# Kernel optimization log

Measured on AMD Instinct MI355X. Metric: run time of the kernel, lower is better.

## Reference

```python
import jax, jax.numpy as jnp
import numpy as np

D_MODEL = 1024
M = 50
B, N = 8, 4096
NOISE_P = 0.0464
TEMP = 0.1
EPS = 1e-12


def _l2norm(v):
    return v / jnp.clip(jnp.linalg.norm(v, axis=-1, keepdims=True), EPS)


def setup_inputs() -> dict:
    key = jax.random.key(0)
    ks = jax.random.split(key, 8)
    x = jax.random.normal(ks[0], (B, N, D_MODEL), dtype=jnp.float32)
    prime_nodes = jax.random.normal(ks[1], (M, D_MODEL), dtype=jnp.float32)
    w_cov = jnp.float32(1.0)
    w_hyd = jnp.float32(0.5)
    w_vdw = jnp.float32(0.1)
    A_cov = jnp.asarray(np.roll(np.eye(M, dtype=np.float32), 1, axis=0))
    A_hyd = jnp.asarray(np.tril(np.ones((M, M), dtype=np.float32), k=-1))
    A_vdw = jax.random.normal(ks[2], (M, M), dtype=jnp.float32) * 0.05
    # expert MLP: Linear(D,4D) -> GELU -> Linear(4D,D); kaiming-uniform-ish init
    lim1 = 1.0 / np.sqrt(D_MODEL)
    lim2 = 1.0 / np.sqrt(4 * D_MODEL)
    W1 = jax.random.uniform(ks[3], (D_MODEL, 4 * D_MODEL), minval=-lim1, maxval=lim1, dtype=jnp.float32)
    b1 = jax.random.uniform(ks[4], (4 * D_MODEL,), minval=-lim1, maxval=lim1, dtype=jnp.float32)
    W2 = jax.random.uniform(ks[5], (4 * D_MODEL, D_MODEL), minval=-lim2, maxval=lim2, dtype=jnp.float32)
    b2 = jax.random.uniform(ks[6], (D_MODEL,), minval=-lim2, maxval=lim2, dtype=jnp.float32)
    return {"x": x, "prime_nodes": prime_nodes, "w_cov": w_cov, "w_hyd": w_hyd,
            "w_vdw": w_vdw, "A_cov": A_cov, "A_hyd": A_hyd, "A_vdw": A_vdw,
            "W1": W1, "b1": b1, "W2": W2, "b2": b2}


def reference(x, prime_nodes, w_cov, w_hyd, w_vdw, A_cov, A_hyd, A_vdw, W1, b1, W2, b2):
    # soft codebook routing: cosine-sim softmax over M primes, temperature 0.1
    C = jax.nn.softmax(jnp.einsum('bnd,md->bnm', _l2norm(x), _l2norm(prime_nodes)) / TEMP, axis=-1)
    H_prime = jnp.einsum('bnm,bnd->bmd', C, x)  # (B, M, D)
    A = jax.nn.softmax(w_cov * A_cov + w_hyd * A_hyd + w_vdw * A_vdw, axis=-1)
    # einsum('mn,bmd->bmd', A, H_prime): n only appears in A -> rowsum scaling
    H = A.sum(axis=1)[None, :, None] * H_prime
    # single latent step (latent_steps=1 default)
    U, _, Vt = jnp.linalg.svd(H, full_matrices=False)  # U:(B,M,M), Vt:(B,M,D)
    H_logic = jnp.einsum('bij,bjd->bid', U, Vt)  # orthogonal (polar) factor
    nk1, nk2 = jax.random.split(jax.random.key(42))
    mask = (jax.random.uniform(nk1, H_logic.shape) < NOISE_P).astype(H_logic.dtype)
    noise = jax.random.normal(nk2, H_logic.shape, dtype=H_logic.dtype) * 0.1
    z = H_logic + mask * noise
    h = jax.nn.gelu(z @ W1 + b1, approximate=False)
    H = jnp.tanh(h @ W2 + b2)
    # residual decode back to tokens (continuous_mode=False)
    return x + jnp.einsum('bnm,bmd->bnd', C, H)
```

## Files before the change

### kernel.cpp

```cpp
#include <hip/hip_runtime.h>
#include <stdint.h>
#include <math.h>

#define NS_ITERS 26
#define PIT 72
#define P2  72

typedef unsigned short u16;
typedef __attribute__((ext_vector_type(8))) short short8;
typedef __attribute__((ext_vector_type(4))) float f32x4;

__device__ __forceinline__ u16 f2b(float f){
  unsigned u = __float_as_uint(f);
  unsigned r = (u + 0x7FFFu + ((u>>16)&1u)) >> 16;
  return (u16)r;
}
__device__ __forceinline__ float b2f(u16 h){ return __uint_as_float(((unsigned)h)<<16); }
__device__ __forceinline__ unsigned pk2(float lo, float hi){
  return (unsigned)f2b(lo) | ((unsigned)f2b(hi) << 16);
}

__host__ __device__ constexpr uint32_t rotl32(uint32_t v, int n){ return (v<<n)|(v>>(32-n)); }
struct TFOut { uint32_t a, b; };
__host__ __device__ constexpr TFOut tf2x32(uint32_t k0, uint32_t k1, uint32_t x0, uint32_t x1){
  uint32_t ks2 = k0 ^ k1 ^ 0x1BD11BDAu;
  x0 += k0; x1 += k1;
#define TFR(R) x0 += x1; x1 = rotl32(x1,(R)) ^ x0;
  TFR(13) TFR(15) TFR(26) TFR(6)
  x0 += k1; x1 += ks2 + 1u;
  TFR(17) TFR(29) TFR(16) TFR(24)
  x0 += ks2; x1 += k0 + 2u;
  TFR(13) TFR(15) TFR(26) TFR(6)
  x0 += k0; x1 += k1 + 3u;
  TFR(17) TFR(29) TFR(16) TFR(24)
  x0 += k1; x1 += ks2 + 4u;
  TFR(13) TFR(15) TFR(26) TFR(6)
  x0 += ks2; x1 += k0 + 5u;
#undef TFR
  return TFOut{x0, x1};
}

__device__ __forceinline__ float erfinv_f32(float x){
  float w = -log1pf(-x*x);
  float p;
  if (w < 5.0f) {
    w -= 2.5f;
    p = 2.81022636e-08f;
    p = fmaf(p, w, 3.43273939e-07f);
    p = fmaf(p, w, -3.5233877e-06f);
    p = fmaf(p, w, -4.39150654e-06f);
    p = fmaf(p, w, 0.00021858087f);
    p = fmaf(p, w, -0.00125372503f);
    p = fmaf(p, w, -0.00417768164f);
    p = fmaf(p, w, 0.246640727f);
    p = fmaf(p, w, 1.50140941f);
  } else {
    w = sqrtf(w) - 3.0f;
    p = -0.000200214257f;
    p = fmaf(p, w, 0.000100950558f);
    p = fmaf(p, w, 0.00134934322f);
    p = fmaf(p, w, -0.00367342844f);
    p = fmaf(p, w, 0.00573950773f);
    p = fmaf(p, w, -0.0076224613f);
    p = fmaf(p, w, 0.00943887047f);
    p = fmaf(p, w, 1.00167406f);
    p = fmaf(p, w, 2.83297682f);
  }
  return p * x;
}

__global__ __launch_bounds__(256) void kprepAll(const float* __restrict__ prime, u16* __restrict__ PT,
                                                const float* __restrict__ W1, u16* __restrict__ W1T,
                                                const float* __restrict__ W2, u16* __restrict__ W2T){
  int blk = blockIdx.x;
  int tid = threadIdx.x;
  if (blk < 64){
    int m = blk;
    u16* dst = PT + m*1024;
    if (m >= 50){ for (int k = tid; k < 1024; k += 256) dst[k] = 0; return; }
    __shared__ float red[256];
    const float* pr = prime + m*1024;
    float ss = 0.f;
    for (int k = tid; k < 1024; k += 256){ float v = pr[k]; ss = fmaf(v,v,ss); }
    red[tid] = ss; __syncthreads();
    for (int s = 128; s > 0; s >>= 1){ if (tid < s) red[tid] += red[tid+s]; __syncthreads(); }
    float sc = 1.0f / fmaxf(sqrtf(red[0]), 1e-12f);
    for (int k = tid; k < 1024; k += 256) dst[k] = f2b(pr[k]*sc);
    return;
  }
  const float* src; u16* dst; int srcStride, dstStride;
  if (blk < 1088){
    int t = blk - 64;
    int kt2 = t >> 6, nt2 = t & 63;
    src = W1 + (size_t)(kt2*64)*4096 + nt2*64; srcStride = 4096;
    dst = W1T + (size_t)(nt2*64)*1024 + kt2*64; dstStride = 1024;
  } else {
    int t = blk - 1088;
    int kt2 = t >> 4, dt2 = t & 15;
    src = W2 + (size_t)(kt2*64)*1024 + dt2*64; srcStride = 1024;
    dst = W2T + (size_t)(dt2*64)*4096 + kt2*64; dstStride = 4096;
  }
  __shared__ __align__(16) u16 ts[64*PIT];
  int r = tid>>2, sseg = tid&3;
  {
    const float* s0 = src + (size_t)r*srcStride + sseg*16;
    unsigned p[8];
#pragma unroll
    for (int i = 0; i < 4; i++){
      float4 v = *reinterpret_cast<const float4*>(s0 + i*4);
      p[2*i]   = pk2(v.x, v.y);
      p[2*i+1] = pk2(v.z, v.w);
    }
    uint4 w0; w0.x=p[0]; w0.y=p[1]; w0.z=p[2]; w0.w=p[3];
    uint4 w1; w1.x=p[4]; w1.y=p[5]; w1.z=p[6]; w1.w=p[7];
    *reinterpret_cast<uint4*>(&ts[r*PIT + sseg*16])     = w0;
    *reinterpret_cast<uint4*>(&ts[r*PIT + sseg*16 + 8]) = w1;
  }
  __syncthreads();
  {
    int n2 = tid>>2, kseg = tid&3;
    unsigned q[8];
#pragma unroll
    for (int j = 0; j < 8; j++){
      u16 lo = ts[(kseg*16 + 2*j)*PIT + n2];
      u16 hi = ts[(kseg*16 + 2*j+1)*PIT + n2];
      q[j] = (unsigned)lo | ((unsigned)hi<<16);
    }
    u16* d2 = dst + (size_t)n2*dstStride + kseg*16;
    uint4 w0; w0.x=q[0]; w0.y=q[1]; w0.z=q[2]; w0.w=q[3];
    uint4 w1; w1.x=q[4]; w1.y=q[5]; w1.z=q[6]; w1.w=q[7];
    *reinterpret_cast<uint4*>(d2)   = w0;
    *reinterpret_cast<uint4*>(d2+8) = w1;
  }
}

__global__ __launch_bounds__(256) void kC(const float* __restrict__ x, const u16* __restrict__ PT,
                                          u16* __restrict__ C, u16* __restrict__ CT){
  int blk = blockIdx.x; int b = blk>>6, n0 = (blk&63)<<6;
  int tid = threadIdx.x, lane = tid&63, w = tid>>6;
  __shared__ __align__(16) u16 xs[64*PIT];
  __shared__ __align__(16) u16 ps[64*PIT];
  __shared__ float sq[64][5];
  f32x4 acc[4] = {{0,0,0,0},{0,0,0,0},{0,0,0,0},{0,0,0,0}};
  float sqa = 0.f;
  int stok = tid>>2, sseg = tid&3;
  int qtok = tid&63, qg = tid>>6;
  const float* xb = x + ((size_t)(b*4096 + n0))*1024;
  for (int kc = 0; kc < 16; kc++){
    int k0 = kc*64;
    __syncthreads();
    {
      const float* src = xb + (size_t)stok*1024 + k0 + sseg*16;
      unsigned p[8];
#pragma unroll
      for (int i = 0; i < 4; i++){
        float4 v = *reinterpret_cast<const float4*>(src + i*4);
        p[2*i]   = pk2(v.x, v.y);
        p[2*i+1] = pk2(v.z, v.w);
      }
      uint4 w0; w0.x=p[0]; w0.y=p[1]; w0.z=p[2]; w0.w=p[3];
      uint4 w1; w1.x=p[4]; w1.y=p[5]; w1.z=p[6]; w1.w=p[7];
      *reinterpret_cast<uint4*>(&xs[stok*PIT + sseg*16])     = w0;
      *reinterpret_cast<uint4*>(&xs[stok*PIT + sseg*16 + 8]) = w1;
    }
    {
      const u16* src = PT + (size_t)stok*1024 + k0 + sseg*16;
      *reinterpret_cast<uint4*>(&ps[stok*PIT + sseg*16])   = *reinterpret_cast<const uint4*>(src);
      *reinterpret_cast<uint4*>(&ps[stok*PIT + sseg*16+8]) = *reinterpret_cast<const uint4*>(src+8);
    }
    __syncthreads();
    {
      const u16* xr = &xs[qtok*PIT + qg*16];
#pragma unroll
      for (int j = 0; j < 16; j++){ float v = b2f(xr[j]); sqa = fmaf(v,v,sqa); }
    }
#pragma unroll
    for (int s = 0; s < 2; s++){
      short8 a = *reinterpret_cast<const short8*>(&xs[(16*w + (lane&15))*PIT + s*32 + (lane>>4)*8]);
#pragma unroll
      for (int t = 0; t < 4; t++){
        short8 bb = *reinterpret_cast<const short8*>(&ps[(t*16 + (lane&15))*PIT + s*32 + (lane>>4)*8]);
        acc[t] = __builtin_amdgcn_mfma_f32_16x16x32_bf16(a, bb, acc[t], 0, 0, 0);
      }
    }
  }
  sq[qtok][qg] = sqa;
  __syncthreads();
  if (tid < 64){
    float ss = sq[tid][0]+sq[tid][1]+sq[tid][2]+sq[tid][3];
    sq[tid][4] = 10.0f / fmaxf(sqrtf(ss), 1e-12f);
  }
  __syncthreads();
  u16* cl = xs;
#pragma unroll
  for (int r = 0; r < 4; r++){
    int gt = 16*w + (lane>>4)*4 + r;
    float scale = sq[gt][4];
    float v[4];
#pragma unroll
    for (int t = 0; t < 4; t++) v[t] = acc[t][r] * scale;
    if ((lane&15) >= 2) v[3] = -1e30f;
    float mx = fmaxf(fmaxf(v[0],v[1]), fmaxf(v[2],v[3]));
#pragma unroll
    for (int off = 1; off < 16; off <<= 1) mx = fmaxf(mx, __shfl_xor(mx, off, 64));
    float e[4], sum = 0.f;
#pragma unroll
    for (int t = 0; t < 4; t++){ e[t] = __expf(v[t]-mx); sum += e[t]; }
#pragma unroll
    for (int off = 1; off < 16; off <<= 1) sum += __shfl_xor(sum, off, 64);
    float inv = 1.0f / sum;
#pragma unroll
    for (int t = 0; t < 4; t++) cl[gt*PIT + t*16 + (lane&15)] = f2b(e[t]*inv);
  }
  __syncthreads();
  {
    u16* dst = C + ((size_t)(b*4096 + n0 + stok))*64 + sseg*16;
    *reinterpret_cast<uint4*>(dst)   = *reinterpret_cast<const uint4*>(&cl[stok*PIT + sseg*16]);
    *reinterpret_cast<uint4*>(dst+8) = *reinterpret_cast<const uint4*>(&cl[stok*PIT + sseg*16+8]);
  }
  {
    int m = tid>>2, nseg = tid&3;
    unsigned vs[8];
#pragma unroll
    for (int j = 0; j < 8; j++){
      u16 lo = cl[(nseg*16 + 2*j)*PIT + m];
      u16 hi = cl[(nseg*16 + 2*j+1)*PIT + m];
      vs[j] = (unsigned)lo | ((unsigned)hi<<16);
    }
    u16* dst = CT + ((size_t)(b*64 + m))*4096 + n0 + nseg*16;
    uint4 w0; w0.x=vs[0]; w0.y=vs[1]; w0.z=vs[2]; w0.w=vs[3];
    uint4 w1; w1.x=vs[4]; w1.y=vs[5]; w1.z=vs[6]; w1.w=vs[7];
    *reinterpret_cast<uint4*>(dst)   = w0;
    *reinterpret_cast<uint4*>(dst+8) = w1;
  }
}

__global__ __launch_bounds__(256) void kHp2(const float* __restrict__ x, const u16* __restrict__ CT,
                                            float* __restrict__ Hpart){
  int blk = blockIdx.x;
  int kt = blk & 3, dt = (blk >> 2) & 15, b = blk >> 6;
  int d0 = dt*64;
  int tid = threadIdx.x, lane = tid&63, w = tid>>6;
  __shared__ __align__(16) u16 cs[64*PIT];
  __shared__ __align__(16) u16 xt[64*PIT];
  f32x4 acc[4] = {{0,0,0,0},{0,0,0,0},{0,0,0,0},{0,0,0,0}};
  int nn = tid>>2, seg = tid&3;
  int np = tid & 31, dsg = tid >> 5;
  for (int nc = 0; nc < 16; nc++){
    int n0 = kt*1024 + nc*64;
    __syncthreads();
    {
      const u16* src = CT + ((size_t)(b*64 + nn))*4096 + n0 + seg*16;
      *reinterpret_cast<uint4*>(&cs[nn*PIT + seg*16])   = *reinterpret_cast<const uint4*>(src);
      *reinterpret_cast<uint4*>(&cs[nn*PIT + seg*16+8]) = *reinterpret_cast<const uint4*>(src+8);
    }
    {
      const float* s0 = x + ((size_t)(b*4096 + n0 + 2*np))*1024 + d0 + dsg*8;
      const float* s1 = s0 + 1024;
      float4 a0 = *reinterpret_cast<const float4*>(s0);
      float4 a1 = *reinterpret_cast<const float4*>(s0+4);
      float4 c0v = *reinterpret_cast<const float4*>(s1);
      float4 c1v = *reinterpret_cast<const float4*>(s1+4);
      float av[8] = {a0.x,a0.y,a0.z,a0.w,a1.x,a1.y,a1.z,a1.w};
      float cv[8] = {c0v.x,c0v.y,c0v.z,c0v.w,c1v.x,c1v.y,c1v.z,c1v.w};
#pragma unroll
      for (int j2 = 0; j2 < 8; j2++){
        int dd = dsg*8 + j2;
        *reinterpret_cast<unsigned*>(&xt[dd*PIT + 2*np]) = pk2(av[j2], cv[j2]);
      }
    }
    __syncthreads();
#pragma unroll
    for (int s = 0; s < 2; s++){
      short8 a = *reinterpret_cast<const short8*>(&cs[(16*w + (lane&15))*PIT + s*32 + (lane>>4)*8]);
#pragma unroll
      for (int t = 0; t < 4; t++){
        short8 bb = *reinterpret_cast<const short8*>(&xt[(t*16 + (lane&15))*PIT + s*32 + (lane>>4)*8]);
        acc[t] = __builtin_amdgcn_mfma_f32_16x16x32_bf16(a, bb, acc[t], 0, 0, 0);
      }
    }
  }
#pragma unroll
  for (int t = 0; t < 4; t++)
#pragma unroll
    for (int r = 0; r < 4; r++){
      int m = 16*w + (lane>>4)*4 + r;
      int d = d0 + t*16 + (lane&15);
      if (m < 50) Hpart[(((size_t)(b*4) + kt)*50 + m)*1024 + d] = acc[t][r];
    }
}

__global__ void kredH(const float* __restrict__ Hpart, float* __restrict__ H, u16* __restrict__ Hb){
  int e = blockIdx.x*256 + threadIdx.x;
  int b = e >> 16, rem = e & 65535;
  int m = rem >> 10, d = rem & 1023;
  size_t o = ((size_t)(b*64 + m))*1024 + d;
  if (m < 50){
    const float* p = Hpart + (size_t)b*204800 + m*1024 + d;
    float s = p[0] + p[51200] + p[102400] + p[153600];
    H[o] = s;
    Hb[o] = f2b(s);
  } else {
    Hb[o] = 0;
  }
}

__global__ __launch_bounds__(256) void kgram(const u16* __restrict__ Hb, float* __restrict__ G){
  int b = blockIdx.x;
  int tid = threadIdx.x, lane = tid&63, w = tid>>6;
  __shared__ __align__(16) u16 hs[64*PIT];
  f32x4 acc[4] = {{0,0,0,0},{0,0,0,0},{0,0,0,0},{0,0,0,0}};
  int m = tid>>2, seg = tid&3;
  for (int kc = 0; kc < 16; kc++){
    int k0 = kc*64;
    __syncthreads();
    const u16* src = Hb + ((size_t)(b*64 + m))*1024 + k0 + seg*16;
    *reinterpret_cast<uint4*>(&hs[m*PIT + seg*16])   = *reinterpret_cast<const uint4*>(src);
    *reinterpret_cast<uint4*>(&hs[m*PIT + seg*16+8]) = *reinterpret_cast<const uint4*>(src+8);
    __syncthreads();
#pragma unroll
    for (int s = 0; s < 2; s++){
      short8 a = *reinterpret_cast<const short8*>(&hs[(16*w + (lane&15))*PIT + s*32 + (lane>>4)*8]);
#pragma unroll
      for (int t = 0; t < 4; t++){
        short8 bb = *reinterpret_cast<const short8*>(&hs[(t*16 + (lane&15))*PIT + s*32 + (lane>>4)*8]);
        acc[t] = __builtin_amdgcn_mfma_f32_16x16x32_bf16(a, bb, acc[t], 0, 0, 0);
      }
    }
  }
#pragma unroll
  for (int t = 0; t < 4; t++)
#pragma unroll
    for (int r = 0; r < 4; r++){
      int i = 16*w + (lane>>4)*4 + r;
      int j = t*16 + (lane&15);
      if (i < 50 && j < 50) G[(size_t)b*2500 + i*50 + j] = acc[t][r];
    }
}

__global__ __launch_bounds__(256) void kns3(const float* __restrict__ G, float* __restrict__ Wm){
  int b = blockIdx.x;
  __shared__ __align__(16) u16 Yr[2][64*P2], Yc[2][64*P2], Zr[2][64*P2], Zc[2][64*P2];
  __shared__ __align__(16) u16 Tr[64*P2], Tc[64*P2];
  __shared__ float sv[2];
  int tid = threadIdx.x, lane = tid&63, w = tid>>6;
  int lr = lane>>4, lc = lane&15;
  int row0 = 16*w;
  const float* Gb = G + (size_t)b*2500;
  if (tid < 64){
    float v = (tid < 50) ? Gb[tid*50+tid] : 0.f;
    for (int off = 1; off < 64; off <<= 1) v += __shfl_xor(v, off, 64);
    if (tid == 0){ sv[0] = 1.0f / v; sv[1] = rsqrtf(v); }
  }
  __syncthreads();
  float rs = sv[0];
  for (int idx = tid; idx < 4096; idx += 256){
    int r = idx>>6, c = idx&63;
    float yv = (r<50 && c<50) ? Gb[r*50+c]*rs : ((r==c) ? 1.f : 0.f);
    float zv = (r==c) ? 1.f : 0.f;
    u16 yb = f2b(yv), zb = f2b(zv);
    Yr[0][r*P2+c] = yb; Yc[0][c*P2+r] = yb;
    Zr[0][r*P2+c] = zb; Zc[0][c*P2+r] = zb;
  }
  __syncthreads();
  for (int it = 0; it < NS_ITERS; it++){
    int cur = it & 1, nxt = cur ^ 1;
    {
      short8 a0 = *reinterpret_cast<const short8*>(&Zr[cur][(row0+lc)*P2 + lr*8]);
      short8 a1 = *reinterpret_cast<const short8*>(&Zr[cur][(row0+lc)*P2 + 32 + lr*8]);
      f32x4 acc[4] = {{0,0,0,0},{0,0,0,0},{0,0,0,0},{0,0,0,0}};
#pragma unroll
      for (int t = 0; t < 4; t++){
        short8 b0 = *reinterpret_cast<const short8*>(&Yc[cur][(t*16+lc)*P2 + lr*8]);
        short8 b1 = *reinterpret_cast<const short8*>(&Yc[cur][(t*16+lc)*P2 + 32 + lr*8]);
        acc[t] = __builtin_amdgcn_mfma_f32_16x16x32_bf16(a0, b0, acc[t], 0, 0, 0);
        acc[t] = __builtin_amdgcn_mfma_f32_16x16x32_bf16(a1, b1, acc[t], 0, 0, 0);
      }
#pragma unroll
      for (int t = 0; t < 4; t++)
#pragma unroll
        for (int r = 0; r < 4; r++){
          int row = row0 + lr*4 + r, col = t*16 + lc;
          float v = ((row==col) ? 1.5f : 0.f) - 0.5f*acc[t][r];
          u16 h = f2b(v);
          Tr[row*P2+col] = h; Tc[col*P2+row] = h;
        }
    }
    __syncthreads();
    {
      short8 ya0 = *reinterpret_cast<const short8*>(&Yr[cur][(row0+lc)*P2 + lr*8]);
      short8 ya1 = *reinterpret_cast<const short8*>(&Yr[cur][(row0+lc)*P2 + 32 + lr*8]);
      short8 ta0 = *reinterpret_cast<const short8*>(&Tr[(row0+lc)*P2 + lr*8]);
      short8 ta1 = *reinterpret_cast<const short8*>(&Tr[(row0+lc)*P2 + 32 + lr*8]);
      f32x4 accY[4] = {{0,0,0,0},{0,0,0,0},{0,0,0,0},{0,0,0,0}};
      f32x4 accZ[4] = {{0,0,0,0},{0,0,0,0},{0,0,0,0},{0,0,0,0}};
#pragma unroll
      for (int t = 0; t < 4; t++){
        short8 tb0 = *reinterpret_cast<const short8*>(&Tc[(t*16+lc)*P2 + lr*8]);
        short8 tb1 = *reinterpret_cast<const short8*>(&Tc[(t*16+lc)*P2 + 32 + lr*8]);
        accY[t] = __builtin_amdgcn_mfma_f32_16x16x32_bf16(ya0, tb0, accY[t], 0, 0, 0);
        accY[t] = __builtin_amdgcn_mfma_f32_16x16x32_bf16(ya1, tb1, accY[t], 0, 0, 0);
        short8 zb0 = *reinterpret_cast<const short8*>(&Zc[cur][(t*16+lc)*P2 + lr*8]);
        short8 zb1 = *reinterpret_cast<const short8*>(&Zc[cur][(t*16+lc)*P2 + 32 + lr*8]);
        accZ[t] = __builtin_amdgcn_mfma_f32_16x16x32_bf16(ta0, zb0, accZ[t], 0, 0, 0);
        accZ[t] = __builtin_amdgcn_mfma_f32_16x16x32_bf16(ta1, zb1, accZ[t], 0, 0, 0);
      }
#pragma unroll
      for (int t = 0; t < 4; t++)
#pragma unroll
        for (int r = 0; r < 4; r++){
          int row = row0 + lr*4 + r, col = t*16 + lc;
          u16 hy = f2b(accY[t][r]);
          u16 hz = f2b(accZ[t][r]);
          Yr[nxt][row*P2+col] = hy; Yc[nxt][col*P2+row] = hy;
          Zr[nxt][row*P2+col] = hz; Zc[nxt][col*P2+row] = hz;
        }
    }
    __syncthreads();
  }
  float rss = sv[1];
  int fin = NS_ITERS & 1;
  for (int idx = tid; idx < 2500; idx += 256){
    int r = idx/50, c = idx - r*50;
    Wm[(size_t)b*2500 + idx] = b2f(Zr[fin][r*P2+c]) * rss;
  }
}

__global__ __launch_bounds__(256) void kapply2(const float* __restrict__ H, const float* __restrict__ Wm,
                                               u16* __restrict__ zb){
  TFOut K1 = tf2x32(0u, 42u, 0u, 0u);
  TFOut K2 = tf2x32(0u, 42u, 0u, 1u);
  int blk = blockIdx.x;
  int dt = blk & 15, b = blk >> 4;
  int d0 = dt*64;
  int tid = threadIdx.x;
  int d = tid & 63, mg = tid >> 6;
  __shared__ __align__(16) float WsT[50*64];
  __shared__ float Hs[50*65];
  for (int idx = tid; idx < 3200; idx += 256){
    int j = idx >> 6, c = idx & 63;
    WsT[idx] = (c < 50) ? Wm[(size_t)b*2500 + c*50 + j] : 0.f;
  }
  for (int idx = tid; idx < 3200; idx += 256){
    int j = idx >> 6, c = idx & 63;
    Hs[j*65 + c] = H[((size_t)(b*64) + j)*1024 + d0 + c];
  }
  __syncthreads();
  float acc[16];
#pragma unroll
  for (int i = 0; i < 16; i++) acc[i] = 0.f;
  for (int j = 0; j < 50; j++){
    float hv = Hs[j*65 + d];
    const float* wb = WsT + j*64 + (mg << 4);
#pragma unroll
    for (int q = 0; q < 4; q++){
      float4 wv = *reinterpret_cast<const float4*>(wb + q*4);
      acc[q*4+0] = fmaf(wv.x, hv, acc[q*4+0]);
      acc[q*4+1] = fmaf(wv.y, hv, acc[q*4+1]);
      acc[q*4+2] = fmaf(wv.z, hv, acc[q*4+2]);
      acc[q*4+3] = fmaf(wv.w, hv, acc[q*4+3]);
    }
  }
#pragma unroll
  for (int i = 0; i < 16; i++){
    int m = (mg << 4) + i;
    size_t zo = ((size_t)(b*64 + m))*1024 + d0 + d;
    u16 ov = 0;
    if (m < 50){
      float val = acc[i];
      uint32_t j = (uint32_t)(((b*50 + m) << 10) + d0 + d);
      TFOut r1 = tf2x32(K1.a, K1.b, 0u, j);
      uint32_t bits = r1.a ^ r1.b;
      float u = __uint_as_float(0x3F800000u | (bits >> 9)) - 1.0f;
      if (u < 0.0464f){
        TFOut r2 = tf2x32(K2.a, K2.b, 0u, j);
        uint32_t nb = r2.a ^ r2.b;
        float ww = __uint_as_float(0x3F800000u | (nb >> 9)) - 1.0f;
        const float lo = -0.99999994f;
        float un = fmaxf(lo, fmaf(ww, 2.0f, lo));
        val += 0.1f * (1.4142135f * erfinv_f32(un));
      }
      ov = f2b(val);
    }
    zb[zo] = ov;
  }
}

__global__ __launch_bounds__(256) void kmlp1(const u16* __restrict__ ZbB, const u16* __restrict__ W1T,
                                             const float* __restrict__ b1, u16* __restrict__ Hh){
  int blk = blockIdx.x; int b = blk>>6, c0 = (blk&63)<<6;
  int tid = threadIdx.x, lane = tid&63, w = tid>>6;
  __shared__ __align__(16) u16 az[64*PIT];
  __shared__ __align__(16) u16 wt[64*PIT];
  f32x4 acc[4] = {{0,0,0,0},{0,0,0,0},{0,0,0,0},{0,0,0,0}};
  int rr = tid>>2, seg = tid&3;
  for (int kc = 0; kc < 16; kc++){
    int k0 = kc*64;
    __syncthreads();
    {
      const u16* src = ZbB + ((size_t)(b*64 + rr))*1024 + k0 + seg*16;
      *reinterpret_cast<uint4*>(&az[rr*PIT + seg*16])   = *reinterpret_cast<const uint4*>(src);
      *reinterpret_cast<uint4*>(&az[rr*PIT + seg*16+8]) = *reinterpret_cast<const uint4*>(src+8);
    }
    {
      const u16* src = W1T + ((size_t)(c0 + rr))*1024 + k0 + seg*16;
      *reinterpret_cast<uint4*>(&wt[rr*PIT + seg*16])   = *reinterpret_cast<const uint4*>(src);
      *reinterpret_cast<uint4*>(&wt[rr*PIT + seg*16+8]) = *reinterpret_cast<const uint4*>(src+8);
    }
    __syncthreads();
#pragma unroll
    for (int s = 0; s < 2; s++){
      short8 a = *reinterpret_cast<const short8*>(&az[(16*w + (lane&15))*PIT + s*32 + (lane>>4)*8]);
#pragma unroll
      for (int t = 0; t < 4; t++){
        short8 bb = *reinterpret_cast<const short8*>(&wt[(t*16 + (lane&15))*PIT + s*32 + (lane>>4)*8]);
        acc[t] = __builtin_amdgcn_mfma_f32_16x16x32_bf16(a, bb, acc[t], 0, 0, 0);
      }
    }
  }
#pragma unroll
  for (int t = 0; t < 4; t++)
#pragma unroll
    for (int r = 0; r < 4; r++){
      int m = 16*w + (lane>>4)*4 + r;
      int n = c0 + t*16 + (lane&15);
      float val = acc[t][r] + b1[n];
      float g = 0.5f * val * (1.0f + erff(val * 0.70710678f));
      Hh[((size_t)(b*64 + m))*4096 + n] = (m < 50) ? f2b(g) : (u16)0;
    }
}

__global__ __launch_bounds__(256) void kmlp2p(const u16* __restrict__ Hh, const u16* __restrict__ W2T,
                                              float* __restrict__ Mpart){
  int blk = blockIdx.x;
  int kt = blk & 3, dt = (blk >> 2) & 15, b = blk >> 6;
  int d0 = dt*64;
  int tid = threadIdx.x, lane = tid&63, w = tid>>6;
  __shared__ __align__(16) u16 az[64*PIT];
  __shared__ __align__(16) u16 wt[64*PIT];
  f32x4 acc[4] = {{0,0,0,0},{0,0,0,0},{0,0,0,0},{0,0,0,0}};
  int rr = tid>>2, seg = tid&3;
  for (int kc = 0; kc < 16; kc++){
    int k0 = kt*1024 + kc*64;
    __syncthreads();
    {
      const u16* src = Hh + ((size_t)(b*64 + rr))*4096 + k0 + seg*16;
      *reinterpret_cast<uint4*>(&az[rr*PIT + seg*16])   = *reinterpret_cast<const uint4*>(src);
      *reinterpret_cast<uint4*>(&az[rr*PIT + seg*16+8]) = *reinterpret_cast<const uint4*>(src+8);
    }
    {
      const u16* src = W2T + ((size_t)(d0 + rr))*4096 + k0 + seg*16;
      *reinterpret_cast<uint4*>(&wt[rr*PIT + seg*16])   = *reinterpret_cast<const uint4*>(src);
      *reinterpret_cast<uint4*>(&wt[rr*PIT + seg*16+8]) = *reinterpret_cast<const uint4*>(src+8);
    }
    __syncthreads();
#pragma unroll
    for (int s = 0; s < 2; s++){
      short8 a = *reinterpret_cast<const short8*>(&az[(16*w + (lane&15))*PIT + s*32 + (lane>>4)*8]);
#pragma unroll
      for (int t = 0; t < 4; t++){
        short8 bb = *reinterpret_cast<const short8*>(&wt[(t*16 + (lane&15))*PIT + s*32 + (lane>>4)*8]);
        acc[t] = __builtin_amdgcn_mfma_f32_16x16x32_bf16(a, bb, acc[t], 0, 0, 0);
      }
    }
  }
#pragma unroll
  for (int t = 0; t < 4; t++)
#pragma unroll
    for (int r = 0; r < 4; r++){
      int m = 16*w + (lane>>4)*4 + r;
      int d = d0 + t*16 + (lane&15);
      if (m < 50) Mpart[(((size_t)(b*4) + kt)*50 + m)*1024 + d] = acc[t][r];
    }
}

__global__ void kredT(const float* __restrict__ Mpart, const float* __restrict__ b2, u16* __restrict__ HfT){
  int e = blockIdx.x*256 + threadIdx.x;
  int b = e >> 16, rem = e & 65535;
  int m = rem >> 10, d = rem & 1023;
  u16 outv = 0;
  if (m < 50){
    const float* p = Mpart + (size_t)b*204800 + m*1024 + d;
    float s = p[0] + p[51200] + p[102400] + p[153600] + b2[d];
    outv = f2b(tanhf(s));
  }
  HfT[((size_t)(b*1024) + d)*64 + m] = outv;
}

__global__ __launch_bounds__(256) void kdec2(const float* __restrict__ x, const u16* __restrict__ C,
                                             const u16* __restrict__ HfT, float* __restrict__ out){
  int blk = blockIdx.x;
  int dq = blk & 3, nt = (blk >> 2) & 63, b = blk >> 8;
  int n0 = nt << 6;
  int tid = threadIdx.x, lane = tid&63, w = tid>>6;
  __shared__ __align__(16) u16 ctile[64*PIT];
  __shared__ __align__(16) u16 htile[64*PIT];
  __shared__ __align__(16) float obuf[64*68];
  int rr = tid>>2, seg = tid&3;
  {
    const u16* src = C + ((size_t)(b*4096 + n0 + rr))*64 + seg*16;
    *reinterpret_cast<uint4*>(&ctile[rr*PIT + seg*16])   = *reinterpret_cast<const uint4*>(src);
    *reinterpret_cast<uint4*>(&ctile[rr*PIT + seg*16+8]) = *reinterpret_cast<const uint4*>(src+8);
  }
  __syncthreads();
  short8 afrag[2];
#pragma unroll
  for (int s = 0; s < 2; s++)
    afrag[s] = *reinterpret_cast<const short8*>(&ctile[(16*w + (lane&15))*PIT + s*32 + (lane>>4)*8]);
  for (int dt2 = 0; dt2 < 4; dt2++){
    int d0 = (dq*4 + dt2) * 64;
    __syncthreads();
    {
      const u16* src = HfT + ((size_t)(b*1024 + d0 + rr))*64 + seg*16;
      *reinterpret_cast<uint4*>(&htile[rr*PIT + seg*16])   = *reinterpret_cast<const uint4*>(src);
      *reinterpret_cast<uint4*>(&htile[rr*PIT + seg*16+8]) = *reinterpret_cast<const uint4*>(src+8);
    }
    __syncthreads();
    f32x4 acc[4] = {{0,0,0,0},{0,0,0,0},{0,0,0,0},{0,0,0,0}};
#pragma unroll
    for (int s = 0; s < 2; s++){
#pragma unroll
      for (int t = 0; t < 4; t++){
        short8 bb = *reinterpret_cast<const short8*>(&htile[(t*16 + (lane&15))*PIT + s*32 + (lane>>4)*8]);
        acc[t] = __builtin_amdgcn_mfma_f32_16x16x32_bf16(afrag[s], bb, acc[t], 0, 0, 0);
      }
    }
#pragma unroll
    for (int t = 0; t < 4; t++)
#pragma unroll
      for (int r = 0; r < 4; r++){
        int nl = 16*w + (lane>>4)*4 + r;
        int dl = t*16 + (lane&15);
        obuf[nl*68 + dl] = acc[t][r];
      }
    __syncthreads();
#pragma unroll
    for (int pass = 0; pass < 4; pass++){
      int s2 = tid + pass*256;
      int nl = s2 >> 4, sg = s2 & 15;
      size_t o = ((size_t)(b*4096 + n0 + nl))*1024 + d0 + sg*4;
      float4 xv = *reinterpret_cast<const float4*>(x + o);
      const float* ob = &obuf[nl*68 + sg*4];
      float4 ov;
      ov.x = xv.x + ob[0];
      ov.y = xv.y + ob[1];
      ov.z = xv.z + ob[2];
      ov.w = xv.w + ob[3];
      *reinterpret_cast<float4*>(out + o) = ov;
    }
  }
}

extern "C" void kernel_launch(void* const* d_in, const int* in_sizes, int n_in,
                              void* d_out, int out_size, void* d_ws, size_t ws_size,
                              hipStream_t stream) {
  (void)in_sizes; (void)n_in; (void)out_size;
  if (ws_size < (size_t)19755264) return;
  const float* x  = (const float*)d_in[0];
  const float* pn = (const float*)d_in[1];
  const float* W1 = (const float*)d_in[8];
  const float* b1 = (const float*)d_in[9];
  const float* W2 = (const float*)d_in[10];
  const float* b2 = (const float*)d_in[11];
  float* out = (float*)d_out;
  char* ws = (char*)d_ws;

  u16*   W1T = (u16*)d_out;
  u16*   W2T = (u16*)d_out + 4194304;

  u16*   C   = (u16*)(ws);
  u16*   CT  = (u16*)(ws + 4194304);
  u16*   ZbB = (u16*)(ws + 4194304 + 1638400);
  u16*   HfT = (u16*)(ws + 4194304 + 2686976);
  u16*   Hh  = (u16*)(ws + 8388608);
  u16*   Hb  = (u16*)(ws + 8388608);
  float* H   = (float*)(ws + 8388608 + 1048576);
  float* HP  = (float*)(ws + 12582912);
  u16*   PT  = (u16*)(ws + 19136512);
  float* G   = (float*)(ws + 19267584);
  float* WM  = (float*)(ws + 19347584);

  hipLaunchKernelGGL(kprepAll, dim3(2112), dim3(256), 0, stream, pn, PT, W1, W1T, W2, W2T);
  hipLaunchKernelGGL(kC,       dim3(512),  dim3(256), 0, stream, x, PT, C, CT);
  hipLaunchKernelGGL(kHp2,     dim3(512),  dim3(256), 0, stream, x, CT, HP);
  hipLaunchKernelGGL(kredH,    dim3(2048), dim3(256), 0, stream, HP, H, Hb);
  hipLaunchKernelGGL(kgram,    dim3(8),    dim3(256), 0, stream, Hb, G);
  hipLaunchKernelGGL(kns3,     dim3(8),    dim3(256), 0, stream, G, WM);
  hipLaunchKernelGGL(kapply2,  dim3(128),  dim3(256), 0, stream, H, WM, ZbB);
  hipLaunchKernelGGL(kmlp1,    dim3(512),  dim3(256), 0, stream, ZbB, W1T, b1, Hh);
  hipLaunchKernelGGL(kmlp2p,   dim3(512),  dim3(256), 0, stream, Hh, W2T, HP);
  hipLaunchKernelGGL(kredT,    dim3(2048), dim3(256), 0, stream, HP, b2, HfT);
  hipLaunchKernelGGL(kdec2,    dim3(2048), dim3(256), 0, stream, x, C, HfT, out);
}
```

Measured before the change: 247.1 us.

## Load MFMA operands directly from global memory in routing kernel, drop LDS staging

The routing-logit kernel now has each lane read its x fragment straight from global memory, convert it to bf16 in registers and feed the MFMA. The prime-node operand is also read directly from global memory instead of being staged through shared memory with two barriers per k-chunk. The squared-norm reduction moves from a shared-memory table to wave shuffles. This removes LDS traffic and block-wide synchronisation from the main loop, at the cost of less coalesced 32-byte-per-lane global reads and no prefetch overlap. The norm is now computed from the fp32 values rather than the bf16-rounded ones.

```diff
diff --git a/kernel.cpp b/kernel.cpp
--- a/kernel.cpp
+++ b/kernel.cpp
@@ -138,64 +138,43 @@
                                           u16* __restrict__ C, u16* __restrict__ CT){
   int blk = blockIdx.x; int b = blk>>6, n0 = (blk&63)<<6;
   int tid = threadIdx.x, lane = tid&63, w = tid>>6;
-  __shared__ __align__(16) u16 xs[64*PIT];
-  __shared__ __align__(16) u16 ps[64*PIT];
-  __shared__ float sq[64][5];
+  __shared__ __align__(16) u16 cl[64*PIT];
   f32x4 acc[4] = {{0,0,0,0},{0,0,0,0},{0,0,0,0},{0,0,0,0}};
   float sqa = 0.f;
-  int stok = tid>>2, sseg = tid&3;
-  int qtok = tid&63, qg = tid>>6;
-  const float* xb = x + ((size_t)(b*4096 + n0))*1024;
+  int tokA = 16*w + (lane&15);
+  int kgrp = lane>>4;
+  const float* xrow = x + ((size_t)(b*4096 + n0 + tokA))*1024;
+  const u16* pbase = PT + (size_t)(lane&15)*1024;
   for (int kc = 0; kc < 16; kc++){
     int k0 = kc*64;
-    __syncthreads();
-    {
-      const float* src = xb + (size_t)stok*1024 + k0 + sseg*16;
-      unsigned p[8];
-#pragma unroll
-      for (int i = 0; i < 4; i++){
-        float4 v = *reinterpret_cast<const float4*>(src + i*4);
-        p[2*i]   = pk2(v.x, v.y);
-        p[2*i+1] = pk2(v.z, v.w);
-      }
-      uint4 w0; w0.x=p[0]; w0.y=p[1]; w0.z=p[2]; w0.w=p[3];
-      uint4 w1; w1.x=p[4]; w1.y=p[5]; w1.z=p[6]; w1.w=p[7];
-      *reinterpret_cast<uint4*>(&xs[stok*PIT + sseg*16])     = w0;
-      *reinterpret_cast<uint4*>(&xs[stok*PIT + sseg*16 + 8]) = w1;
-    }
-    {
-      const u16* src = PT + (size_t)stok*1024 + k0 + sseg*16;
-      *reinterpret_cast<uint4*>(&ps[stok*PIT + sseg*16])   = *reinterpret_cast<const uint4*>(src);
-      *reinterpret_cast<uint4*>(&ps[stok*PIT + sseg*16+8]) = *reinterpret_cast<const uint4*>(src+8);
-    }
-    __syncthreads();
-    {
-      const u16* xr = &xs[qtok*PIT + qg*16];
-#pragma unroll
-      for (int j = 0; j < 16; j++){ float v = b2f(xr[j]); sqa = fmaf(v,v,sqa); }
-    }
 #pragma unroll
     for (int s = 0; s < 2; s++){
-      short8 a = *reinterpret_cast<const short8*>(&xs[(16*w + (lane&15))*PIT + s*32 + (lane>>4)*8]);
-#pragma unroll
-      for (int t = 0; t < 4; t++){
-        short8 bb = *reinterpret_cast<const short8*>(&ps[(t*16 + (lane&15))*PIT + s*32 + (lane>>4)*8]);
+      int kk = k0 + s*32 + kgrp*8;
+      float4 v0 = *reinterpret_cast<const float4*>(xrow + kk);
+      float4 v1 = *reinterpret_cast<const float4*>(xrow + kk + 4);
+      sqa = fmaf(v0.x,v0.x,sqa); sqa = fmaf(v0.y,v0.y,sqa);
+      sqa = fmaf(v0.z,v0.z,sqa); sqa = fmaf(v0.w,v0.w,sqa);
+      sqa = fmaf(v1.x,v1.x,sqa); sqa = fmaf(v1.y,v1.y,sqa);
+      sqa = fmaf(v1.z,v1.z,sqa); sqa = fmaf(v1.w,v1.w,sqa);
+      union { unsigned u[4]; short8 s8; } cv;
+      cv.u[0] = pk2(v0.x, v0.y); cv.u[1] = pk2(v0.z, v0.w);
+      cv.u[2] = pk2(v1.x, v1.y); cv.u[3] = pk2(v1.z, v1.w);
+      short8 a = cv.s8;
+#pragma unroll
+      for (int t = 0; t < 4; t++){
+        short8 bb = *reinterpret_cast<const short8*>(pbase + (size_t)t*16*1024 + kk);
         acc[t] = __builtin_amdgcn_mfma_f32_16x16x32_bf16(a, bb, acc[t], 0, 0, 0);
       }
     }
   }
-  sq[qtok][qg] = sqa;
-  __syncthreads();
-  if (tid < 64){
-    float ss = sq[tid][0]+sq[tid][1]+sq[tid][2]+sq[tid][3];
-    sq[tid][4] = 10.0f / fmaxf(sqrtf(ss), 1e-12f);
-  }
-  __syncthreads();
-  u16* cl = xs;
+  sqa += __shfl_xor(sqa, 16, 64);
+  sqa += __shfl_xor(sqa, 32, 64);
+  float inorm = 10.0f / fmaxf(sqrtf(sqa), 1e-12f);
 #pragma unroll
   for (int r = 0; r < 4; r++){
-    int gt = 16*w + (lane>>4)*4 + r;
-    float scale = sq[gt][4];
+    int tl = (lane>>4)*4 + r;
+    int gt = 16*w + tl;
+    float scale = __shfl(inorm, tl, 64);
     float v[4];
 #pragma unroll
     for (int t = 0; t < 4; t++) v[t] = acc[t][r] * scale;
@@ -213,6 +192,7 @@
     for (int t = 0; t < 4; t++) cl[gt*PIT + t*16 + (lane&15)] = f2b(e[t]*inv);
   }
   __syncthreads();
+  int stok = tid>>2, sseg = tid&3;
   {
     u16* dst = C + ((size_t)(b*4096 + n0 + stok))*64 + sseg*16;
     *reinterpret_cast<uint4*>(dst)   = *reinterpret_cast<const uint4*>(&cl[stok*PIT + sseg*16]);
```

Measured after the change: 258.5 us. 1.05x slower.
